# Kernel optimization log

Hardware: AMD Instinct MI355X
Metric: run time of the kernel (lower is better)

## Reference

```python
import jax, jax.numpy as jnp
import numpy as np

# dims (match init_kwargs)
N, M = 128, 2048
DX, DY, DU, DZ = 64, 8, 256, 256
EPS = 0.01


def setup_inputs() -> dict:
    key = jax.random.key(0)
    kit = iter(jax.random.split(key, 40))
    def w(*shape):
        fan_in = shape[-1]
        return jax.random.normal(next(kit), shape, jnp.float32) / np.float32(np.sqrt(fan_in))
    def b(*shape):
        return 0.1 * jax.random.normal(next(kit), shape, jnp.float32)
    inp = {
        'X_tensor': jax.random.normal(next(kit), (N, DX), jnp.float32),
        'U_tensor': jax.random.normal(next(kit), (M, DY), jnp.float32),
        'Y_tensor': jax.random.normal(next(kit), (N, DY), jnp.float32),
        # context path (x -> u_i)
        'Wt0': w(DU, DX), 'bt0': b(DU),
        'Wt1': w(DU, DU), 'bt1': b(DU),
        # PICNN cell 0 (input cell, no z term)
        'Wyu0': w(DY, DX), 'byu0': b(DY), 'Wy0': w(DZ, DY), 'Wu0': w(DZ, DX), 'b0': b(DZ),
        # PICNN cell 1 (hidden cell, nonneg Wz1 via softplus)
        'Wzu1': w(DZ, DU), 'bzu1': b(DZ), 'Wz1': w(DZ, DZ),
        'Wyu1': w(DY, DU), 'byu1': b(DY), 'Wy1': w(DZ, DY), 'Wu1': w(DZ, DU), 'b1': b(DZ),
        # PICNN cell 2 (output cell, scalar potential)
        'Wzu2': w(DZ, DU), 'bzu2': b(DZ), 'Wz2': w(1, DZ),
        'Wyu2': w(DY, DU), 'byu2': b(DY), 'Wy2': w(1, DY), 'Wu2': w(1, DU), 'b2': b(1),
    }
    return inp


def _psi(X, U, Y, Wt0, bt0, Wt1, bt1, Wyu0, byu0, Wy0, Wu0, b0,
         Wzu1, bzu1, Wz1, Wyu1, byu1, Wy1, Wu1, b1,
         Wzu2, bzu2, Wz2, Wyu2, byu2, Wy2, Wu2, b2):
    relu = jax.nn.relu
    # context path depends only on X -> compute once per row, broadcast over m samples
    u1 = relu(X @ Wt0.T + bt0)                       # [n, du]
    u2 = relu(u1 @ Wt1.T + bt1)                      # [n, du]
    # cell 0: z1 [n, m, dz]  (pairwise over X rows x U samples)
    gy0 = X @ Wyu0.T + byu0                          # [n, dy]
    z1 = relu(jnp.einsum('md,nd,zd->nmz', U, gy0, Wy0)
              + (X @ Wu0.T + b0)[:, None, :])
    # cell 1: hidden convex cell with nonneg z-weight
    gz1 = relu(u1 @ Wzu1.T + bzu1)                   # [n, dz]
    gy1 = u1 @ Wyu1.T + byu1                         # [n, dy]
    z2 = relu(jnp.einsum('nmz,nz,kz->nmk', z1, gz1, jax.nn.softplus(Wz1))
              + jnp.einsum('md,nd,kd->nmk', U, gy1, Wy1)
              + (u1 @ Wu1.T + b1)[:, None, :])       # [n, m, dz]
    # output cell -> scalar potential phi(x_i, u_j)
    gz2 = relu(u2 @ Wzu2.T + bzu2)                   # [n, dz]
    gy2 = u2 @ Wyu2.T + byu2                         # [n, dy]
    phi = (jnp.einsum('nmz,nz,z->nm', z2, gz2, jax.nn.softplus(Wz2)[0])
           + jnp.einsum('md,nd,d->nm', U, gy2, Wy2[0])
           + (u2 @ Wu2[0] + b2[0])[:, None])         # [n, m]
    # entropic OT dual psi with stable row-wise logsumexp
    cost = Y @ U.T                                   # [n, m]
    slack = cost - phi
    row_max = jnp.max(slack, axis=1, keepdims=True)
    log_mean_exp = (jax.nn.logsumexp((slack - row_max) / EPS, axis=1, keepdims=True)
                    - jnp.log(jnp.float32(slack.shape[1])))
    return EPS * (log_mean_exp + row_max / EPS)      # [n, 1]


def reference(X_tensor, U_tensor, Y_tensor, Wt0, bt0, Wt1, bt1, Wyu0, byu0, Wy0, Wu0, b0,
              Wzu1, bzu1, Wz1, Wyu1, byu1, Wy1, Wu1, b1,
              Wzu2, bzu2, Wz2, Wyu2, byu2, Wy2, Wu2, b2):
    return _psi(X_tensor, U_tensor, Y_tensor, Wt0, bt0, Wt1, bt1, Wyu0, byu0, Wy0, Wu0, b0,
                Wzu1, bzu1, Wz1, Wyu1, byu1, Wy1, Wu1, b1,
                Wzu2, bzu2, Wz2, Wyu2, byu2, Wy2, Wu2, b2)
```

## Files before the change

### kernel.cpp

```cpp
#include <hip/hip_runtime.h>

#define NN 128
#define MM 2048
#define EPSF 0.01f

typedef __bf16 bf16x8 __attribute__((ext_vector_type(8)));
typedef __bf16 bf16x4 __attribute__((ext_vector_type(4)));
typedef float  f32x4  __attribute__((ext_vector_type(4)));

#define WS_SLACK 0
#define WS_WT1F  0
#define WS_WZU1F 32768
#define WS_WU1F  65536
#define WS_WZU2F 98304
#define WS_WT0F  131072
#define WS_WU0F  139264
#define WS_XF    147456
#define WS_W2    262144
#define WS_GZ1   294912
#define WS_YV    327680
#define WS_CU2   328704
#define WS_WTF   328832
#define WS_A2    361600
#define WS_B2    394368
#define WS_BX    918656

__device__ __forceinline__ float softplusf(float x) {
    return x > 20.f ? x : log1pf(expf(x));
}

__device__ __forceinline__ bf16x8 ld_cvt8(const float* __restrict__ p) {
    const float4* p4 = (const float4*)p;
    float4 a = p4[0], b = p4[1];
    bf16x8 r;
    r[0] = (__bf16)a.x; r[1] = (__bf16)a.y; r[2] = (__bf16)a.z; r[3] = (__bf16)a.w;
    r[4] = (__bf16)b.x; r[5] = (__bf16)b.y; r[6] = (__bf16)b.z; r[7] = (__bf16)b.w;
    return r;
}

template<int CH, bool SP>
__device__ __forceinline__ void frag_cvt(const float* __restrict__ W,
                                         __bf16* __restrict__ F, int o) {
    const int j0 = o & 7;
    const int lane = (o >> 3) & 63;
    const int c = lane & 15, q = lane >> 4;
    const int ch = (o >> 9) & (CH - 1);
    const int ot = o >> (CH == 8 ? 12 : 10);
    const float* src = W + (ot * 16 + c) * (CH * 32) + ch * 32 + q * 8 + j0;
    float4 v = *(const float4*)src;
    bf16x4 r;
    if (SP) {
        r[0] = (__bf16)softplusf(v.x); r[1] = (__bf16)softplusf(v.y);
        r[2] = (__bf16)softplusf(v.z); r[3] = (__bf16)softplusf(v.w);
    } else {
        r[0] = (__bf16)v.x; r[1] = (__bf16)v.y;
        r[2] = (__bf16)v.z; r[3] = (__bf16)v.w;
    }
    *(bf16x4*)(F + o) = r;
}

__global__ __launch_bounds__(256) void k_wprep(
    const float* __restrict__ X, const float* __restrict__ U,
    const float* __restrict__ Wt0, const float* __restrict__ Wu0,
    const float* __restrict__ Wt1, const float* __restrict__ Wzu1,
    const float* __restrict__ Wu1, const float* __restrict__ Wzu2,
    const float* __restrict__ Wz1,
    float* __restrict__ ws)
{
    const int b = blockIdx.x, t = threadIdx.x;
    if (b < 64) {
        frag_cvt<8, true>(Wz1, (__bf16*)(ws + WS_WTF), b * 1024 + t * 4);
    } else if (b < 128) {
        const int i = (b - 64) * 1024 + t * 4;
        const int m = i >> 5, cc = i & 31;
        bf16x4 r;
        if (cc < 8) {
            float4 u = *(const float4*)(U + m * 8 + cc);
            r[0] = (__bf16)u.x; r[1] = (__bf16)u.y;
            r[2] = (__bf16)u.z; r[3] = (__bf16)u.w;
        } else if (cc == 8) {
            r[0] = (__bf16)1.f; r[1] = (__bf16)0.f; r[2] = (__bf16)0.f; r[3] = (__bf16)0.f;
        } else {
            r[0] = (__bf16)0.f; r[1] = (__bf16)0.f; r[2] = (__bf16)0.f; r[3] = (__bf16)0.f;
        }
        *(bf16x4*)((__bf16*)(ws + WS_A2) + i) = r;
    } else if (b < 192) {
        frag_cvt<8, false>(Wt1, (__bf16*)(ws + WS_WT1F), (b - 128) * 1024 + t * 4);
    } else if (b < 256) {
        frag_cvt<8, false>(Wzu1, (__bf16*)(ws + WS_WZU1F), (b - 192) * 1024 + t * 4);
    } else if (b < 320) {
        frag_cvt<8, false>(Wu1, (__bf16*)(ws + WS_WU1F), (b - 256) * 1024 + t * 4);
    } else if (b < 384) {
        frag_cvt<8, false>(Wzu2, (__bf16*)(ws + WS_WZU2F), (b - 320) * 1024 + t * 4);
    } else if (b < 400) {
        frag_cvt<2, false>(Wt0, (__bf16*)(ws + WS_WT0F), (b - 384) * 1024 + t * 4);
    } else if (b < 416) {
        frag_cvt<2, false>(Wu0, (__bf16*)(ws + WS_WU0F), (b - 400) * 1024 + t * 4);
    } else {
        frag_cvt<2, false>(X, (__bf16*)(ws + WS_XF), (b - 416) * 1024 + t * 4);
    }
}

__global__ __launch_bounds__(512) void k_ctx4(
    const float* __restrict__ Y,
    const float* __restrict__ bt0, const float* __restrict__ b0,
    const float* __restrict__ Wyu0, const float* __restrict__ byu0,
    const float* __restrict__ Wy0,
    const float* __restrict__ bt1, const float* __restrict__ bzu1,
    const float* __restrict__ Wyu1, const float* __restrict__ byu1,
    const float* __restrict__ Wy1,
    const float* __restrict__ b1,
    const float* __restrict__ bzu2, const float* __restrict__ Wz2,
    const float* __restrict__ Wyu2, const float* __restrict__ byu2,
    const float* __restrict__ Wy2, const float* __restrict__ b2,
    float* __restrict__ ws)
{
    __shared__ __bf16 u1b[16][264];
    __shared__ __bf16 u2b[16][264];
    __shared__ __bf16 c0q[16][64];
    __shared__ __bf16 c1q[16][64];
    __shared__ float gy0s[16][8];
    __shared__ float gy1s[16][8];

    const int t = threadIdx.x, b = blockIdx.x;
    const int w = t >> 6, lane = t & 63;
    const int c = lane & 15, q = lane >> 4;
    const int g = b >> 2, s = b & 3;
    const int nb = g * 16;

    const __bf16* Xf    = (const __bf16*)(ws + WS_XF);
    const __bf16* Wt0f  = (const __bf16*)(ws + WS_WT0F);
    const __bf16* Wu0f  = (const __bf16*)(ws + WS_WU0F);
    const __bf16* Wt1f  = (const __bf16*)(ws + WS_WT1F);
    const __bf16* Wzu1f = (const __bf16*)(ws + WS_WZU1F);
    const __bf16* Wu1f  = (const __bf16*)(ws + WS_WU1F);
    const __bf16* Wzu2f = (const __bf16*)(ws + WS_WZU2F);

    bf16x8 a1[2];
#pragma unroll
    for (int ch = 0; ch < 2; ++ch)
        a1[ch] = *(const bf16x8*)(Xf + ((g * 2 + ch) * 64 + lane) * 8);

    for (int tt = w; tt < 16; tt += 8) {
        f32x4 D = {0.f, 0.f, 0.f, 0.f};
#pragma unroll
        for (int ch = 0; ch < 2; ++ch) {
            bf16x8 bb = *(const bf16x8*)(Wt0f + ((tt * 2 + ch) * 64 + lane) * 8);
            D = __builtin_amdgcn_mfma_f32_16x16x32_bf16(a1[ch], bb, D, 0, 0, 0);
        }
        const float bv = bt0[tt * 16 + c];
#pragma unroll
        for (int r = 0; r < 4; ++r)
            u1b[4 * q + r][tt * 16 + c] = (__bf16)fmaxf(D[r] + bv, 0.f);
    }
    if (w < 4) {
        const int ot = 4 * s + w;
        f32x4 D = {0.f, 0.f, 0.f, 0.f};
#pragma unroll
        for (int ch = 0; ch < 2; ++ch) {
            bf16x8 bb = *(const bf16x8*)(Wu0f + ((ot * 2 + ch) * 64 + lane) * 8);
            D = __builtin_amdgcn_mfma_f32_16x16x32_bf16(a1[ch], bb, D, 0, 0, 0);
        }
        const float bv = b0[ot * 16 + c];
#pragma unroll
        for (int r = 0; r < 4; ++r)
            c0q[4 * q + r][w * 16 + c] = (__bf16)(D[r] + bv);
    } else if (w == 4) {
        const float* rp = Wyu0 + (c & 7) * 64;
        f32x4 D = {0.f, 0.f, 0.f, 0.f};
#pragma unroll
        for (int ch = 0; ch < 2; ++ch) {
            bf16x8 bb = ld_cvt8(rp + ch * 32 + q * 8);
            D = __builtin_amdgcn_mfma_f32_16x16x32_bf16(a1[ch], bb, D, 0, 0, 0);
        }
        if (c < 8) {
            const float bv = byu0[c];
#pragma unroll
            for (int r = 0; r < 4; ++r)
                gy0s[4 * q + r][c] = D[r] + bv;
        }
    }
    __syncthreads();

    bf16x8 aF[8];
#pragma unroll
    for (int ch = 0; ch < 8; ++ch)
        aF[ch] = *(const bf16x8*)&u1b[c][ch * 32 + q * 8];

    for (int tt = w; tt < 16; tt += 8) {
        f32x4 D = {0.f, 0.f, 0.f, 0.f};
#pragma unroll
        for (int ch = 0; ch < 8; ++ch) {
            bf16x8 bb = *(const bf16x8*)(Wt1f + ((tt * 8 + ch) * 64 + lane) * 8);
            D = __builtin_amdgcn_mfma_f32_16x16x32_bf16(aF[ch], bb, D, 0, 0, 0);
        }
        const float bv = bt1[tt * 16 + c];
#pragma unroll
        for (int r = 0; r < 4; ++r)
            u2b[4 * q + r][tt * 16 + c] = (__bf16)fmaxf(D[r] + bv, 0.f);
    }
    if (w < 4) {
        const int ot = 4 * s + w, col = ot * 16 + c;
        f32x4 D = {0.f, 0.f, 0.f, 0.f};
#pragma unroll
        for (int ch = 0; ch < 8; ++ch) {
            bf16x8 bb = *(const bf16x8*)(Wzu1f + ((ot * 8 + ch) * 64 + lane) * 8);
            D = __builtin_amdgcn_mfma_f32_16x16x32_bf16(aF[ch], bb, D, 0, 0, 0);
        }
        const float bv = bzu1[col];
#pragma unroll
        for (int r = 0; r < 4; ++r)
            ws[WS_GZ1 + (nb + 4 * q + r) * 256 + col] = fmaxf(D[r] + bv, 0.f);
    } else {
        const int ot = 4 * s + (w - 4);
        f32x4 D = {0.f, 0.f, 0.f, 0.f};
#pragma unroll
        for (int ch = 0; ch < 8; ++ch) {
            bf16x8 bb = *(const bf16x8*)(Wu1f + ((ot * 8 + ch) * 64 + lane) * 8);
            D = __builtin_amdgcn_mfma_f32_16x16x32_bf16(aF[ch], bb, D, 0, 0, 0);
        }
        const float bv = b1[ot * 16 + c];
#pragma unroll
        for (int r = 0; r < 4; ++r)
            c1q[4 * q + r][(w - 4) * 16 + c] = (__bf16)(D[r] + bv);
    }
    if (w == 0) {
        const float* rp = Wyu1 + (c & 7) * 256;
        f32x4 D = {0.f, 0.f, 0.f, 0.f};
#pragma unroll
        for (int ch = 0; ch < 8; ++ch) {
            bf16x8 bb = ld_cvt8(rp + ch * 32 + q * 8);
            D = __builtin_amdgcn_mfma_f32_16x16x32_bf16(aF[ch], bb, D, 0, 0, 0);
        }
        if (c < 8) {
            const float bv = byu1[c];
#pragma unroll
            for (int r = 0; r < 4; ++r)
                gy1s[4 * q + r][c] = D[r] + bv;
        }
    }
    __syncthreads();

    bf16x8 aG[8];
#pragma unroll
    for (int ch = 0; ch < 8; ++ch)
        aG[ch] = *(const bf16x8*)&u2b[c][ch * 32 + q * 8];

    if (w < 4) {
        const int ot = 4 * s + w, col = ot * 16 + c;
        f32x4 D = {0.f, 0.f, 0.f, 0.f};
#pragma unroll
        for (int ch = 0; ch < 8; ++ch) {
            bf16x8 bb = *(const bf16x8*)(Wzu2f + ((ot * 8 + ch) * 64 + lane) * 8);
            D = __builtin_amdgcn_mfma_f32_16x16x32_bf16(aG[ch], bb, D, 0, 0, 0);
        }
        const float bv = bzu2[col];
        const float sp = softplusf(Wz2[col]);
#pragma unroll
        for (int r = 0; r < 4; ++r) {
            float gz2 = fmaxf(D[r] + bv, 0.f);
            ws[WS_W2 + (nb + 4 * q + r) * 256 + col] = gz2 * sp;
        }
    } else if (w == 4 && s == 0) {
        const float* rp = (c < 8) ? (Wyu2 + c * 256) : Wyu2;
        if (c >= 8) rp = (const float*)Wz2;
        rp = (c < 8) ? (Wyu2 + c * 256) : ((const float*)0);
        ;
        f32x4 D = {0.f, 0.f, 0.f, 0.f};
        const float* rpp = (c < 8) ? (Wyu2 + c * 256) : (byu2 - byu2 + (const float*)nullptr);
        (void)rp; (void)rpp;
        D = f32x4{0.f, 0.f, 0.f, 0.f};
        const float* rr = (c < 8) ? (Wyu2 + c * 256) : nullptr;
        (void)rr;
        ;
    }
    if (w == 4 && s == 0) {
        extern const float* __yv_dummy;
    }
    {
    }
    if (w == 5 && s == 0) { }

    if (w == 4 && s == 0) {
    }

    {
        bf16x8 zz;
#pragma unroll
        for (int j = 0; j < 8; ++j) zz[j] = (__bf16)0.f;
#pragma unroll
        for (int j = 0; j < 2; ++j) {
            const int idx = j * 512 + t;
            const int zl = idx & 63, nl = idx >> 6;
            const int z = 64 * s + zl, n = nb + nl;
            {
                const float* wy = Wy0 + z * 8;
                __bf16* dst = (__bf16*)(ws + WS_B2) + (n * 256 + z) * 32;
                bf16x8 v0, v1 = zz;
#pragma unroll
                for (int d = 0; d < 8; ++d) v0[d] = (__bf16)(gy0s[nl][d] * wy[d]);
                v1[0] = c0q[nl][zl];
                *(bf16x8*)(dst)      = v0;
                *(bf16x8*)(dst + 8)  = v1;
                *(bf16x8*)(dst + 16) = zz;
                *(bf16x8*)(dst + 24) = zz;
            }
            {
                const float* wy = Wy1 + z * 8;
                __bf16* dst = (__bf16*)(ws + WS_BX) + (n * 256 + z) * 32;
                bf16x8 v0, v1 = zz;
#pragma unroll
                for (int d = 0; d < 8; ++d) v0[d] = (__bf16)(gy1s[nl][d] * wy[d]);
                v1[0] = c1q[nl][zl];
                *(bf16x8*)(dst)      = v0;
                *(bf16x8*)(dst + 8)  = v1;
                *(bf16x8*)(dst + 16) = zz;
                *(bf16x8*)(dst + 24) = zz;
            }
        }
    }
}


__global__ __launch_bounds__(256, 4) void k_main(
    const float* __restrict__ U,
    float* __restrict__ ws)
{
    __shared__ __bf16 zh[64][264];
    __shared__ float gz1s[256];
    __shared__ float w2s[256];
    __shared__ float sdot[64];
    __shared__ float psum[4][64];

    const int t  = threadIdx.x;
    const int n  = blockIdx.y;
    const int m0 = blockIdx.x * 64;
    const int w    = t >> 6;
    const int lane = t & 63;
    const int c = lane & 15;
    const int q = lane >> 4;

    gz1s[t] = ws[WS_GZ1 + n * 256 + t];
    w2s[t]  = ws[WS_W2  + n * 256 + t];
    if (t < 64) {
        float sd = 0.f;
#pragma unroll
        for (int d = 0; d < 8; ++d)
            sd += U[(m0 + t) * 8 + d] * ws[WS_YV + n * 8 + d];
        sdot[t] = sd;
    }

    const __bf16* A2p = (const __bf16*)(ws + WS_A2);
    const __bf16* B2p = (const __bf16*)(ws + WS_B2) + n * 8192;
    const __bf16* BXp = (const __bf16*)(ws + WS_BX) + n * 8192;
    const __bf16* WTF = (const __bf16*)(ws + WS_WTF);

    bf16x8 a2f[4];
#pragma unroll
    for (int mi = 0; mi < 4; ++mi)
        a2f[mi] = *(const bf16x8*)(A2p + (m0 + 16 * mi + c) * 32 + q * 8);

    {
        bf16x8 b2f[4];
#pragma unroll
        for (int zt = 0; zt < 4; ++zt)
            b2f[zt] = *(const bf16x8*)(B2p + (64 * w + 16 * zt + c) * 32 + q * 8);
        f32x4 pre[4][4];
#pragma unroll
        for (int zt = 0; zt < 4; ++zt)
#pragma unroll
            for (int mi = 0; mi < 4; ++mi) {
                f32x4 zacc = {0.f, 0.f, 0.f, 0.f};
                pre[zt][mi] = __builtin_amdgcn_mfma_f32_16x16x32_bf16(
                    b2f[zt], a2f[mi], zacc, 0, 0, 0);
            }
#pragma unroll
        for (int zt = 0; zt < 4; ++zt) {
            const int zb = 64 * w + 16 * zt + 4 * q;
#pragma unroll
            for (int mi = 0; mi < 4; ++mi) {
                bf16x4 v4;
#pragma unroll
                for (int r = 0; r < 4; ++r)
                    v4[r] = (__bf16)(fmaxf(pre[zt][mi][r], 0.f) * gz1s[zb + r]);
                *(bf16x4*)&zh[c + 16 * mi][zb] = v4;
            }
        }
    }

    f32x4 acc[4][4];
#pragma unroll
    for (int mi = 0; mi < 4; ++mi)
#pragma unroll
        for (int kj = 0; kj < 4; ++kj)
            acc[mi][kj] = f32x4{0.f, 0.f, 0.f, 0.f};

    __syncthreads();

    for (int ch = 0; ch < 8; ++ch) {
        bf16x8 az[4], bw[4];
#pragma unroll
        for (int mi = 0; mi < 4; ++mi)
            az[mi] = *(const bf16x8*)&zh[c + 16 * mi][ch * 32 + q * 8];
#pragma unroll
        for (int kj = 0; kj < 4; ++kj)
            bw[kj] = *(const bf16x8*)(WTF + ((4 * w + kj) * 8 + ch) * 512 + lane * 8);
#pragma unroll
        for (int mi = 0; mi < 4; ++mi)
#pragma unroll
            for (int kj = 0; kj < 4; ++kj)
                acc[mi][kj] = __builtin_amdgcn_mfma_f32_16x16x32_bf16(
                    az[mi], bw[kj], acc[mi][kj], 0, 0, 0);
    }
    {
        bf16x8 bx[4];
#pragma unroll
        for (int kj = 0; kj < 4; ++kj)
            bx[kj] = *(const bf16x8*)(BXp + (64 * w + 16 * kj + c) * 32 + q * 8);
#pragma unroll
        for (int mi = 0; mi < 4; ++mi)
#pragma unroll
            for (int kj = 0; kj < 4; ++kj)
                acc[mi][kj] = __builtin_amdgcn_mfma_f32_16x16x32_bf16(
                    a2f[mi], bx[kj], acc[mi][kj], 0, 0, 0);
    }

    float p[4][4];
#pragma unroll
    for (int mi = 0; mi < 4; ++mi)
#pragma unroll
        for (int r = 0; r < 4; ++r) p[mi][r] = 0.f;
#pragma unroll
    for (int kj = 0; kj < 4; ++kj) {
        float w2v = w2s[64 * w + 16 * kj + c];
#pragma unroll
        for (int mi = 0; mi < 4; ++mi)
#pragma unroll
            for (int r = 0; r < 4; ++r)
                p[mi][r] += fmaxf(acc[mi][kj][r], 0.f) * w2v;
    }
#pragma unroll
    for (int mi = 0; mi < 4; ++mi)
#pragma unroll
        for (int r = 0; r < 4; ++r) {
            float v = p[mi][r];
            v += __shfl_xor(v, 8);
            v += __shfl_xor(v, 4);
            v += __shfl_xor(v, 2);
            v += __shfl_xor(v, 1);
            p[mi][r] = v;
        }
    if (c == 0) {
#pragma unroll
        for (int mi = 0; mi < 4; ++mi)
            *(float4*)&psum[w][16 * mi + 4 * q] =
                make_float4(p[mi][0], p[mi][1], p[mi][2], p[mi][3]);
    }
    __syncthreads();
    if (t < 64) {
        float cu2 = ws[WS_CU2 + n];
        float pp = psum[0][t] + psum[1][t] + psum[2][t] + psum[3][t];
        ws[WS_SLACK + n * 2048 + m0 + t] = sdot[t] - cu2 - pp;
    }
}

__global__ __launch_bounds__(256) void k_lse(const float* __restrict__ ws,
                                             float* __restrict__ out) {
    __shared__ float redmax[4];
    __shared__ float redsum[4];
    const int n = blockIdx.x;
    const int t = threadIdx.x;
    const float* s = ws + WS_SLACK + n * 2048;

    float vals[8];
    float mx = -3.4e38f;
#pragma unroll
    for (int i = 0; i < 8; ++i) {
        vals[i] = s[t + 256 * i];
        mx = fmaxf(mx, vals[i]);
    }
#pragma unroll
    for (int off = 32; off; off >>= 1) mx = fmaxf(mx, __shfl_xor(mx, off));
    if ((t & 63) == 0) redmax[t >> 6] = mx;
    __syncthreads();
    mx = fmaxf(fmaxf(redmax[0], redmax[1]), fmaxf(redmax[2], redmax[3]));

    float sum = 0.f;
#pragma unroll
    for (int i = 0; i < 8; ++i) sum += expf((vals[i] - mx) * (1.f / EPSF));
#pragma unroll
    for (int off = 32; off; off >>= 1) sum += __shfl_xor(sum, off);
    if ((t & 63) == 0) redsum[t >> 6] = sum;
    __syncthreads();
    if (t == 0) {
        float S = redsum[0] + redsum[1] + redsum[2] + redsum[3];
        out[n] = EPSF * logf(S * (1.f / 2048.f)) + mx;
    }
}

__global__ __launch_bounds__(256) void k_yvcu(
    const float* __restrict__ Y,
    const float* __restrict__ bt0, const float* __restrict__ bt1,
    const float* __restrict__ Wyu2, const float* __restrict__ byu2,
    const float* __restrict__ Wy2,
    const float* __restrict__ Wu2, const float* __restrict__ b2,
    float* __restrict__ ws)
{
    __shared__ __bf16 u1b[16][264];
    __shared__ __bf16 u2b[16][264];
    const int t = threadIdx.x, g = blockIdx.x;
    const int w = t >> 6, lane = t & 63;
    const int c = lane & 15, q = lane >> 4;
    const int nb = g * 16;

    const __bf16* Xf   = (const __bf16*)(ws + WS_XF);
    const __bf16* Wt0f = (const __bf16*)(ws + WS_WT0F);
    const __bf16* Wt1f = (const __bf16*)(ws + WS_WT1F);

    bf16x8 a1[2];
#pragma unroll
    for (int ch = 0; ch < 2; ++ch)
        a1[ch] = *(const bf16x8*)(Xf + ((g * 2 + ch) * 64 + lane) * 8);
    for (int tt = w; tt < 16; tt += 4) {
        f32x4 D = {0.f, 0.f, 0.f, 0.f};
#pragma unroll
        for (int ch = 0; ch < 2; ++ch) {
            bf16x8 bb = *(const bf16x8*)(Wt0f + ((tt * 2 + ch) * 64 + lane) * 8);
            D = __builtin_amdgcn_mfma_f32_16x16x32_bf16(a1[ch], bb, D, 0, 0, 0);
        }
        const float bv = bt0[tt * 16 + c];
#pragma unroll
        for (int r = 0; r < 4; ++r)
            u1b[4 * q + r][tt * 16 + c] = (__bf16)fmaxf(D[r] + bv, 0.f);
    }
    __syncthreads();

    bf16x8 aF[8];
#pragma unroll
    for (int ch = 0; ch < 8; ++ch)
        aF[ch] = *(const bf16x8*)&u1b[c][ch * 32 + q * 8];
    for (int tt = w; tt < 16; tt += 4) {
        f32x4 D = {0.f, 0.f, 0.f, 0.f};
#pragma unroll
        for (int ch = 0; ch < 8; ++ch) {
            bf16x8 bb = *(const bf16x8*)(Wt1f + ((tt * 8 + ch) * 64 + lane) * 8);
            D = __builtin_amdgcn_mfma_f32_16x16x32_bf16(aF[ch], bb, D, 0, 0, 0);
        }
        const float bv = bt1[tt * 16 + c];
#pragma unroll
        for (int r = 0; r < 4; ++r)
            u2b[4 * q + r][tt * 16 + c] = (__bf16)fmaxf(D[r] + bv, 0.f);
    }
    __syncthreads();

    if (w == 0) {
        bf16x8 aG[8];
#pragma unroll
        for (int ch = 0; ch < 8; ++ch)
            aG[ch] = *(const bf16x8*)&u2b[c][ch * 32 + q * 8];
        const float* rp = (c < 8) ? (Wyu2 + c * 256) : Wu2;
        f32x4 D = {0.f, 0.f, 0.f, 0.f};
#pragma unroll
        for (int ch = 0; ch < 8; ++ch) {
            bf16x8 bb = ld_cvt8(rp + ch * 32 + q * 8);
            D = __builtin_amdgcn_mfma_f32_16x16x32_bf16(aG[ch], bb, D, 0, 0, 0);
        }
        if (c < 8) {
            const float bv = byu2[c];
            const float wy2 = Wy2[c];
#pragma unroll
            for (int r = 0; r < 4; ++r) {
                const int n = nb + 4 * q + r;
                ws[WS_YV + n * 8 + c] = Y[n * 8 + c] - (D[r] + bv) * wy2;
            }
        } else if (c == 8) {
#pragma unroll
            for (int r = 0; r < 4; ++r)
                ws[WS_CU2 + nb + 4 * q + r] = D[r] + b2[0];
        }
    }
}

extern "C" void kernel_launch(void* const* d_in, const int* in_sizes, int n_in,
                              void* d_out, int out_size, void* d_ws, size_t ws_size,
                              hipStream_t stream) {
    const float* X    = (const float*)d_in[0];
    const float* Uu   = (const float*)d_in[1];
    const float* Yy   = (const float*)d_in[2];
    const float* Wt0  = (const float*)d_in[3];
    const float* bt0  = (const float*)d_in[4];
    const float* Wt1  = (const float*)d_in[5];
    const float* bt1  = (const float*)d_in[6];
    const float* Wyu0 = (const float*)d_in[7];
    const float* byu0 = (const float*)d_in[8];
    const float* Wy0  = (const float*)d_in[9];
    const float* Wu0  = (const float*)d_in[10];
    const float* b0   = (const float*)d_in[11];
    const float* Wzu1 = (const float*)d_in[12];
    const float* bzu1 = (const float*)d_in[13];
    const float* Wz1  = (const float*)d_in[14];
    const float* Wyu1 = (const float*)d_in[15];
    const float* byu1 = (const float*)d_in[16];
    const float* Wy1  = (const float*)d_in[17];
    const float* Wu1  = (const float*)d_in[18];
    const float* b1   = (const float*)d_in[19];
    const float* Wzu2 = (const float*)d_in[20];
    const float* bzu2 = (const float*)d_in[21];
    const float* Wz2  = (const float*)d_in[22];
    const float* Wyu2 = (const float*)d_in[23];
    const float* byu2 = (const float*)d_in[24];
    const float* Wy2  = (const float*)d_in[25];
    const float* Wu2  = (const float*)d_in[26];
    const float* b2   = (const float*)d_in[27];
    float* ws  = (float*)d_ws;
    float* out = (float*)d_out;

    k_wprep<<<dim3(424), dim3(256), 0, stream>>>(
        X, Uu, Wt0, Wu0, Wt1, Wzu1, Wu1, Wzu2, Wz1, ws);
    k_ctx4<<<dim3(32), dim3(512), 0, stream>>>(
        Yy, bt0, b0, Wyu0, byu0, Wy0, bt1, bzu1, Wyu1, byu1, Wy1, b1,
        bzu2, Wz2, Wyu2, byu2, Wy2, b2, ws);
    k_yvcu<<<dim3(8), dim3(256), 0, stream>>>(
        Yy, bt0, bt1, Wyu2, byu2, Wy2, Wu2, b2, ws);
    k_main<<<dim3(MM / 64, NN), dim3(256), 0, stream>>>(Uu, ws);
    k_lse<<<dim3(128), dim3(256), 0, stream>>>(ws, out);
}
```

Measured before the change: 176.4 us.

## Fold yv/cu2 computation into context kernel and split main launch in two

Moves the Wyu2/Wu2 projection that produced the yv and cu2 values from the separate k_yvcu kernel into an otherwise idle wave of k_ctx, which removes one kernel launch and the recomputation of u1/u2. The main pairwise kernel is also split into two launches over halves of the M dimension using an m_base offset. The split adds a launch and a tail gap between the halves, and its purpose is unclear.

```diff
diff --git a/kernel.cpp b/kernel.cpp
--- a/kernel.cpp
+++ b/kernel.cpp
@@ -101,7 +101,7 @@
     }
 }
 
-__global__ __launch_bounds__(512) void k_ctx4(
+__global__ __launch_bounds__(512) void k_ctx(
     const float* __restrict__ Y,
     const float* __restrict__ bt0, const float* __restrict__ b0,
     const float* __restrict__ Wyu0, const float* __restrict__ byu0,
@@ -112,7 +112,8 @@
     const float* __restrict__ b1,
     const float* __restrict__ bzu2, const float* __restrict__ Wz2,
     const float* __restrict__ Wyu2, const float* __restrict__ byu2,
-    const float* __restrict__ Wy2, const float* __restrict__ b2,
+    const float* __restrict__ Wy2,
+    const float* __restrict__ Wu2, const float* __restrict__ b2,
     float* __restrict__ ws)
 {
     __shared__ __bf16 u1b[16][264];
@@ -262,26 +263,26 @@
             ws[WS_W2 + (nb + 4 * q + r) * 256 + col] = gz2 * sp;
         }
     } else if (w == 4 && s == 0) {
-        const float* rp = (c < 8) ? (Wyu2 + c * 256) : Wyu2;
-        if (c >= 8) rp = (const float*)Wz2;
-        rp = (c < 8) ? (Wyu2 + c * 256) : ((const float*)0);
-        ;
-        f32x4 D = {0.f, 0.f, 0.f, 0.f};
-        const float* rpp = (c < 8) ? (Wyu2 + c * 256) : (byu2 - byu2 + (const float*)nullptr);
-        (void)rp; (void)rpp;
-        D = f32x4{0.f, 0.f, 0.f, 0.f};
-        const float* rr = (c < 8) ? (Wyu2 + c * 256) : nullptr;
-        (void)rr;
-        ;
-    }
-    if (w == 4 && s == 0) {
-        extern const float* __yv_dummy;
-    }
-    {
-    }
-    if (w == 5 && s == 0) { }
-
-    if (w == 4 && s == 0) {
+        const float* rp = (c < 8) ? (Wyu2 + c * 256) : Wu2;
+        f32x4 D = {0.f, 0.f, 0.f, 0.f};
+#pragma unroll
+        for (int ch = 0; ch < 8; ++ch) {
+            bf16x8 bb = ld_cvt8(rp + ch * 32 + q * 8);
+            D = __builtin_amdgcn_mfma_f32_16x16x32_bf16(aG[ch], bb, D, 0, 0, 0);
+        }
+        if (c < 8) {
+            const float bv = byu2[c];
+            const float wy2 = Wy2[c];
+#pragma unroll
+            for (int r = 0; r < 4; ++r) {
+                const int n = nb + 4 * q + r;
+                ws[WS_YV + n * 8 + c] = Y[n * 8 + c] - (D[r] + bv) * wy2;
+            }
+        } else if (c == 8) {
+#pragma unroll
+            for (int r = 0; r < 4; ++r)
+                ws[WS_CU2 + nb + 4 * q + r] = D[r] + b2[0];
+        }
     }
 
     {
@@ -321,10 +322,10 @@
     }
 }
 
-
 __global__ __launch_bounds__(256, 4) void k_main(
     const float* __restrict__ U,
-    float* __restrict__ ws)
+    float* __restrict__ ws,
+    int m_base)
 {
     __shared__ __bf16 zh[64][264];
     __shared__ float gz1s[256];
@@ -334,7 +335,7 @@
 
     const int t  = threadIdx.x;
     const int n  = blockIdx.y;
-    const int m0 = blockIdx.x * 64;
+    const int m0 = (blockIdx.x + m_base) * 64;
     const int w    = t >> 6;
     const int lane = t & 63;
     const int c = lane & 15;
@@ -495,89 +496,6 @@
     if (t == 0) {
         float S = redsum[0] + redsum[1] + redsum[2] + redsum[3];
         out[n] = EPSF * logf(S * (1.f / 2048.f)) + mx;
-    }
-}
-
-__global__ __launch_bounds__(256) void k_yvcu(
-    const float* __restrict__ Y,
-    const float* __restrict__ bt0, const float* __restrict__ bt1,
-    const float* __restrict__ Wyu2, const float* __restrict__ byu2,
-    const float* __restrict__ Wy2,
-    const float* __restrict__ Wu2, const float* __restrict__ b2,
-    float* __restrict__ ws)
-{
-    __shared__ __bf16 u1b[16][264];
-    __shared__ __bf16 u2b[16][264];
-    const int t = threadIdx.x, g = blockIdx.x;
-    const int w = t >> 6, lane = t & 63;
-    const int c = lane & 15, q = lane >> 4;
-    const int nb = g * 16;
-
-    const __bf16* Xf   = (const __bf16*)(ws + WS_XF);
-    const __bf16* Wt0f = (const __bf16*)(ws + WS_WT0F);
-    const __bf16* Wt1f = (const __bf16*)(ws + WS_WT1F);
-
-    bf16x8 a1[2];
-#pragma unroll
-    for (int ch = 0; ch < 2; ++ch)
-        a1[ch] = *(const bf16x8*)(Xf + ((g * 2 + ch) * 64 + lane) * 8);
-    for (int tt = w; tt < 16; tt += 4) {
-        f32x4 D = {0.f, 0.f, 0.f, 0.f};
-#pragma unroll
-        for (int ch = 0; ch < 2; ++ch) {
-            bf16x8 bb = *(const bf16x8*)(Wt0f + ((tt * 2 + ch) * 64 + lane) * 8);
-            D = __builtin_amdgcn_mfma_f32_16x16x32_bf16(a1[ch], bb, D, 0, 0, 0);
-        }
-        const float bv = bt0[tt * 16 + c];
-#pragma unroll
-        for (int r = 0; r < 4; ++r)
-            u1b[4 * q + r][tt * 16 + c] = (__bf16)fmaxf(D[r] + bv, 0.f);
-    }
-    __syncthreads();
-
-    bf16x8 aF[8];
-#pragma unroll
-    for (int ch = 0; ch < 8; ++ch)
-        aF[ch] = *(const bf16x8*)&u1b[c][ch * 32 + q * 8];
-    for (int tt = w; tt < 16; tt += 4) {
-        f32x4 D = {0.f, 0.f, 0.f, 0.f};
-#pragma unroll
-        for (int ch = 0; ch < 8; ++ch) {
-            bf16x8 bb = *(const bf16x8*)(Wt1f + ((tt * 8 + ch) * 64 + lane) * 8);
-            D = __builtin_amdgcn_mfma_f32_16x16x32_bf16(aF[ch], bb, D, 0, 0, 0);
-        }
-        const float bv = bt1[tt * 16 + c];
-#pragma unroll
-        for (int r = 0; r < 4; ++r)
-            u2b[4 * q + r][tt * 16 + c] = (__bf16)fmaxf(D[r] + bv, 0.f);
-    }
-    __syncthreads();
-
-    if (w == 0) {
-        bf16x8 aG[8];
-#pragma unroll
-        for (int ch = 0; ch < 8; ++ch)
-            aG[ch] = *(const bf16x8*)&u2b[c][ch * 32 + q * 8];
-        const float* rp = (c < 8) ? (Wyu2 + c * 256) : Wu2;
-        f32x4 D = {0.f, 0.f, 0.f, 0.f};
-#pragma unroll
-        for (int ch = 0; ch < 8; ++ch) {
-            bf16x8 bb = ld_cvt8(rp + ch * 32 + q * 8);
-            D = __builtin_amdgcn_mfma_f32_16x16x32_bf16(aG[ch], bb, D, 0, 0, 0);
-        }
-        if (c < 8) {
-            const float bv = byu2[c];
-            const float wy2 = Wy2[c];
-#pragma unroll
-            for (int r = 0; r < 4; ++r) {
-                const int n = nb + 4 * q + r;
-                ws[WS_YV + n * 8 + c] = Y[n * 8 + c] - (D[r] + bv) * wy2;
-            }
-        } else if (c == 8) {
-#pragma unroll
-            for (int r = 0; r < 4; ++r)
-                ws[WS_CU2 + nb + 4 * q + r] = D[r] + b2[0];
-        }
     }
 }
 
@@ -617,11 +535,10 @@
 
     k_wprep<<<dim3(424), dim3(256), 0, stream>>>(
         X, Uu, Wt0, Wu0, Wt1, Wzu1, Wu1, Wzu2, Wz1, ws);
-    k_ctx4<<<dim3(32), dim3(512), 0, stream>>>(
+    k_ctx<<<dim3(32), dim3(512), 0, stream>>>(
         Yy, bt0, b0, Wyu0, byu0, Wy0, bt1, bzu1, Wyu1, byu1, Wy1, b1,
-        bzu2, Wz2, Wyu2, byu2, Wy2, b2, ws);
-    k_yvcu<<<dim3(8), dim3(256), 0, stream>>>(
-        Yy, bt0, bt1, Wyu2, byu2, Wy2, Wu2, b2, ws);
-    k_main<<<dim3(MM / 64, NN), dim3(256), 0, stream>>>(Uu, ws);
+        bzu2, Wz2, Wyu2, byu2, Wy2, Wu2, b2, ws);
+    k_main<<<dim3(16, NN), dim3(256), 0, stream>>>(Uu, ws, 0);
+    k_main<<<dim3(16, NN), dim3(256), 0, stream>>>(Uu, ws, 16);
     k_lse<<<dim3(128), dim3(256), 0, stream>>>(ws, out);
 }
```

Result: no change. 172.9 us (median of 2 runs) (-2.0%).
